# Performance work log

Measured on AMD Instinct MI355X. Metric: run time of the kernel, lower is better.

The kernel has to match this reference:

```python
import jax, jax.numpy as jnp
import numpy as np

B, N, E = 1024, 40, 64
P = N * (N - 1) // 2  # 780 field pairs


def _pair_indices(n):
    row, col = [], []
    for i in range(n - 1):
        for j in range(i + 1, n):
            row.append(i)
            col.append(j)
    return np.asarray(row), np.asarray(col)


def setup_inputs() -> dict:
    key = jax.random.key(0)
    k1, k2 = jax.random.split(key)
    inputs = jax.random.normal(k1, (B, N, E), dtype=jnp.float32)
    # xavier-normal-ish init for the 'mat' kernel (E, P, E)
    std = float(np.sqrt(2.0 / (E + E)))
    param = jax.random.normal(k2, (E, P, E), dtype=jnp.float32) * std
    return {"inputs": inputs, "param": param}


def reference(inputs, param):
    n = inputs.shape[1]
    rowidx, colidx = _pair_indices(n)
    p = inputs[:, rowidx]  # (B, P, E)
    q = inputs[:, colidx]  # (B, P, E)
    # torch: kp = (p[:,None] * param).sum(-1).transpose(1,2); out = (kp*q).sum(-1)
    # == out[b,i] = sum_{e,f} p[b,i,e] * param[f,i,e] * q[b,i,f]
    out = jnp.einsum('bie,fie,bif->bi', p, param, q)
    return out[:, None, :]  # (B, 1, P)
```

## Files before the change

### kernel.cpp

```cpp
#include <hip/hip_runtime.h>

namespace {
constexpr int kB = 1024;
constexpr int kN = 40;
constexpr int kE = 64;
constexpr int kP = kN * (kN - 1) / 2;

using bf16x8 = __attribute__((ext_vector_type(8))) short;
using f32x4  = __attribute__((ext_vector_type(4))) float;

__device__ inline unsigned short f2bf(float x) {
  union { float f; unsigned u; } v; v.f = x;
  return (unsigned short)((v.u + 0x7FFFu + ((v.u >> 16) & 1u)) >> 16);
}
__device__ inline float bf2f(unsigned short u) {
  union { unsigned u; float f; } v; v.u = (unsigned)u << 16;
  return v.f;
}

__global__ __launch_bounds__(256) void prep(const float* __restrict__ in,
                                            const float* __restrict__ param,
                                            unsigned short* __restrict__ xf,
                                            unsigned short* __restrict__ Af) {
  __shared__ short Ms[64 * 72];
  const int t = threadIdx.x;
  if (blockIdx.x < 640) {
    const int n    = blockIdx.x >> 4;
    const int bgc  = blockIdx.x & 15;
    const int bgl  = t >> 6;
    const int L    = t & 63;
    const int col  = L & 15;
    const int quad = L >> 4;
    const int b    = (bgc * 4 + bgl) * 16 + col;
    const float* src    = in + ((size_t)b * kN + n) * kE + quad * 8;
    unsigned short* dst = xf + (((size_t)n * 64 + bgc * 4 + bgl) << 10) + L * 8;
    const float4 v0 = ((const float4*)src)[0];
    const float4 v1 = ((const float4*)src)[1];
    const float4 v2 = ((const float4*)(src + 32))[0];
    const float4 v3 = ((const float4*)(src + 32))[1];
    bf16x8 o0, o1;
    o0[0] = (short)f2bf(v0.x); o0[1] = (short)f2bf(v0.y);
    o0[2] = (short)f2bf(v0.z); o0[3] = (short)f2bf(v0.w);
    o0[4] = (short)f2bf(v1.x); o0[5] = (short)f2bf(v1.y);
    o0[6] = (short)f2bf(v1.z); o0[7] = (short)f2bf(v1.w);
    o1[0] = (short)f2bf(v2.x); o1[1] = (short)f2bf(v2.y);
    o1[2] = (short)f2bf(v2.z); o1[3] = (short)f2bf(v2.w);
    o1[4] = (short)f2bf(v3.x); o1[5] = (short)f2bf(v3.y);
    o1[6] = (short)f2bf(v3.z); o1[7] = (short)f2bf(v3.w);
    *(bf16x8*)dst         = o0;
    *(bf16x8*)(dst + 512) = o1;
  } else {
    const int i = blockIdx.x - 640;
#pragma unroll
    for (int ph = 0; ph < 4; ++ph) {
      const int f  = ph * 16 + (t >> 4);
      const int e0 = (t & 15) * 4;
      const float4 v = *(const float4*)(param + ((size_t)f * kP + i) * kE + e0);
      short* d = &Ms[f * 72 + e0];
      d[0] = (short)f2bf(v.x); d[1] = (short)f2bf(v.y);
      d[2] = (short)f2bf(v.z); d[3] = (short)f2bf(v.w);
    }
    __syncthreads();
    unsigned short* base = Af + (size_t)i * 4096;
#pragma unroll
    for (int u = 0; u < 2; ++u) {
      const int chunk = t * 2 + u;
      const int L    = chunk & 63;
      const int mtks = chunk >> 6;
      const int mt   = mtks >> 1, ks = mtks & 1;
      const int col  = L & 15, quad = L >> 4;
      const bf16x8 a = *(const bf16x8*)&Ms[(16 * mt + col) * 72 + ks * 32 + quad * 8];
      *(bf16x8*)(base + chunk * 8) = a;
    }
  }
}

__global__ __launch_bounds__(256, 4)
void opn_pair2(const unsigned short* __restrict__ xf,
               const unsigned short* __restrict__ Af,
               float* __restrict__ out) {
  __shared__ float dots[256 * 2];

  const int t    = threadIdx.x;
  const int w    = t >> 6;
  const int L    = t & 63;
  const int col  = L & 15;
  const int quad = L >> 4;

  int tx = blockIdx.x, r = 0;
  for (;;) { const int nq = (40 - r) >> 1; if (tx < nq) break; tx -= nq; ++r; }
  const int c0  = r + 1 + tx * 2;
  const int ib  = r * (79 - r) / 2 + c0 - r - 1;
  const int gb0 = blockIdx.y * 256;

  const int cc = w & 1;
  const int h  = w >> 1;
  const int c  = c0 + cc;

  if (c <= kN - 1) {
    const unsigned short* ab = Af + (size_t)(ib + cc) * 4096 + L * 8;
    bf16x8 A[4][2];
#pragma unroll
    for (int mt = 0; mt < 4; ++mt)
#pragma unroll
      for (int ks = 0; ks < 2; ++ks)
        A[mt][ks] = *(const bf16x8*)(ab + (mt * 2 + ks) * 512);

    const int bgg0 = blockIdx.y * 16 + h * 8;
    const unsigned short* pb = xf + (((size_t)r * 64 + bgg0) << 10);
    const unsigned short* qb = xf + (((size_t)c * 64 + bgg0) << 10);
    const int qoff = (quad >> 1) * 128 + col * 8 + (quad & 1) * 4;

    bf16x8 B0[2], B1[2];
    ushort4 Q[2][4];
    B0[0]   = *(const bf16x8*)(pb + L * 8);
    B1[0]   = *(const bf16x8*)(pb + 512 + L * 8);
    Q[0][0] = *(const ushort4*)(qb + qoff);
    Q[0][1] = *(const ushort4*)(qb + 256 + qoff);
    Q[0][2] = *(const ushort4*)(qb + 512 + qoff);
    Q[0][3] = *(const ushort4*)(qb + 768 + qoff);

#pragma unroll
    for (int bg = 0; bg < 8; ++bg) {
      const int cb = bg & 1, nb = cb ^ 1;
      if (bg < 7) {
        const unsigned short* pn = pb + ((size_t)(bg + 1) << 10);
        const unsigned short* qn = qb + ((size_t)(bg + 1) << 10);
        B0[nb]   = *(const bf16x8*)(pn + L * 8);
        B1[nb]   = *(const bf16x8*)(pn + 512 + L * 8);
        Q[nb][0] = *(const ushort4*)(qn + qoff);
        Q[nb][1] = *(const ushort4*)(qn + 256 + qoff);
        Q[nb][2] = *(const ushort4*)(qn + 512 + qoff);
        Q[nb][3] = *(const ushort4*)(qn + 768 + qoff);
      }
      f32x4 acc[4];
#pragma unroll
      for (int mt = 0; mt < 4; ++mt) acc[mt] = (f32x4){0.f, 0.f, 0.f, 0.f};
#pragma unroll
      for (int mt = 0; mt < 4; ++mt) {
        acc[mt] = __builtin_amdgcn_mfma_f32_16x16x32_bf16(A[mt][0], B0[cb], acc[mt], 0, 0, 0);
        acc[mt] = __builtin_amdgcn_mfma_f32_16x16x32_bf16(A[mt][1], B1[cb], acc[mt], 0, 0, 0);
      }
      float s[4];
#pragma unroll
      for (int mt = 0; mt < 4; ++mt) {
        const ushort4 qu = Q[cb][mt];
        float sm;
        sm = acc[mt][0] * bf2f(qu.x);
        sm = fmaf(acc[mt][1], bf2f(qu.y), sm);
        sm = fmaf(acc[mt][2], bf2f(qu.z), sm);
        sm = fmaf(acc[mt][3], bf2f(qu.w), sm);
        s[mt] = sm;
      }
      float dot = (s[0] + s[1]) + (s[2] + s[3]);
      dot += __shfl_xor(dot, 16, 64);
      dot += __shfl_xor(dot, 32, 64);
      if (quad == 0) dots[(h * 128 + bg * 16 + col) * 2 + cc] = dot;
    }
  }
  __syncthreads();

  const float2 dv = *(const float2*)&dots[t * 2];
  float* ob = out + (size_t)(gb0 + t) * kP + ib;
  ob[0] = dv.x;
  if (c0 + 1 <= kN - 1) ob[1] = dv.y;
}

__global__ __launch_bounds__(256, 2)
void opn_fp32(const float* __restrict__ inp, const float* __restrict__ param,
              float* __restrict__ out) {
  const int i    = blockIdx.x;
  const int wave = threadIdx.x >> 6;
  const int lane = threadIdx.x & 63;
  const int b    = (blockIdx.y * 4 + wave) * 64 + lane;
  int rem = i, r = 0;
  while (rem >= kN - 1 - r) { rem -= kN - 1 - r; ++r; }
  const int c = r + 1 + rem;
  const float* pb = inp + (size_t)b * (kN * kE) + r * kE;
  const float* qb = inp + (size_t)b * (kN * kE) + c * kE;
  float p[kE];
#pragma unroll
  for (int e = 0; e < kE; ++e) p[e] = pb[e];
  float acc = 0.f;
  for (int f = 0; f < kE; ++f) {
    const float* Mrow = param + ((size_t)f * kP + i) * kE;
    float t0 = 0.f, t1 = 0.f, t2 = 0.f, t3 = 0.f;
#pragma unroll
    for (int e = 0; e < kE; e += 4) {
      t0 = fmaf(Mrow[e + 0], p[e + 0], t0);
      t1 = fmaf(Mrow[e + 1], p[e + 1], t1);
      t2 = fmaf(Mrow[e + 2], p[e + 2], t2);
      t3 = fmaf(Mrow[e + 3], p[e + 3], t3);
    }
    acc = fmaf((t0 + t1) + (t2 + t3), qb[f], acc);
  }
  out[(size_t)b * kP + i] = acc;
}
}

extern "C" void kernel_launch(void* const* d_in, const int* in_sizes, int n_in,
                              void* d_out, int out_size, void* d_ws, size_t ws_size,
                              hipStream_t stream) {
  const float* inputs = (const float*)d_in[0];
  const float* param  = (const float*)d_in[1];
  float* out          = (float*)d_out;

  const size_t xf_bytes = (size_t)kN * kB * kE * sizeof(unsigned short);
  const size_t af_bytes = (size_t)kP * 4096 * sizeof(unsigned short);

  if (ws_size >= xf_bytes + af_bytes) {
    unsigned short* xf = (unsigned short*)d_ws;
    unsigned short* Af = (unsigned short*)((char*)d_ws + xf_bytes);
    prep<<<640 + kP, 256, 0, stream>>>(inputs, param, xf, Af);
    opn_pair2<<<dim3(400, 4), 256, 0, stream>>>(xf, Af, out);
  } else {
    opn_fp32<<<dim3(kP, 4), 256, 0, stream>>>(inputs, param, out);
  }
}
```

Measured before the change: 89.38 us.

## Tile pairs as 2x4 row/column blocks per workgroup for operand reuse

The main kernel now gives each 512-thread workgroup a 2-row by 4-column tile of field pairs, one wave per pair, with each wave covering all 256 batch rows of its y-block. Before, a workgroup handled two adjacent columns of one row and split the batch range across wave halves. The aim is to let the eight waves share the same p and q field slices through cache, to cut launch count (110x4 instead of 400x4), and to write several outputs per row. In exchange, waves whose pair falls on or below the diagonal do no work, each wave runs a longer serial loop of 16 batch groups, and there are fewer workgroups to spread across the GPU.

```diff
diff --git a/kernel.cpp b/kernel.cpp
--- a/kernel.cpp
+++ b/kernel.cpp
@@ -75,11 +75,11 @@
   }
 }
 
-__global__ __launch_bounds__(256, 4)
-void opn_pair2(const unsigned short* __restrict__ xf,
+__global__ __launch_bounds__(512, 4)
+void opn_tile2(const unsigned short* __restrict__ xf,
                const unsigned short* __restrict__ Af,
                float* __restrict__ out) {
-  __shared__ float dots[256 * 2];
+  __shared__ float dots[2][256][4];
 
   const int t    = threadIdx.x;
   const int w    = t >> 6;
@@ -87,18 +87,19 @@
   const int col  = L & 15;
   const int quad = L >> 4;
 
-  int tx = blockIdx.x, r = 0;
-  for (;;) { const int nq = (40 - r) >> 1; if (tx < nq) break; tx -= nq; ++r; }
-  const int c0  = r + 1 + tx * 2;
-  const int ib  = r * (79 - r) / 2 + c0 - r - 1;
+  int a = 0, tx = blockIdx.x;
+  for (;;) { const int nb = 10 - ((2 * a + 1) >> 2); if (tx < nb) break; tx -= nb; ++a; }
+  const int cb  = ((2 * a + 1) >> 2) + tx;
+  const int r0  = 2 * a, c0 = 4 * cb;
   const int gb0 = blockIdx.y * 256;
 
-  const int cc = w & 1;
-  const int h  = w >> 1;
-  const int c  = c0 + cc;
-
-  if (c <= kN - 1) {
-    const unsigned short* ab = Af + (size_t)(ib + cc) * 4096 + L * 8;
+  const int rr = w >> 2, cc = w & 3;
+  const int r = r0 + rr, c = c0 + cc;
+
+  if (c > r) {
+    const int i = r * (79 - r) / 2 + c - r - 1;
+
+    const unsigned short* ab = Af + (size_t)i * 4096 + L * 8;
     bf16x8 A[4][2];
 #pragma unroll
     for (int mt = 0; mt < 4; ++mt)
@@ -106,7 +107,7 @@
       for (int ks = 0; ks < 2; ++ks)
         A[mt][ks] = *(const bf16x8*)(ab + (mt * 2 + ks) * 512);
 
-    const int bgg0 = blockIdx.y * 16 + h * 8;
+    const int bgg0 = blockIdx.y * 16;
     const unsigned short* pb = xf + (((size_t)r * 64 + bgg0) << 10);
     const unsigned short* qb = xf + (((size_t)c * 64 + bgg0) << 10);
     const int qoff = (quad >> 1) * 128 + col * 8 + (quad & 1) * 4;
@@ -121,30 +122,30 @@
     Q[0][3] = *(const ushort4*)(qb + 768 + qoff);
 
 #pragma unroll
-    for (int bg = 0; bg < 8; ++bg) {
-      const int cb = bg & 1, nb = cb ^ 1;
-      if (bg < 7) {
+    for (int bg = 0; bg < 16; ++bg) {
+      const int cbi = bg & 1, nbi = cbi ^ 1;
+      if (bg < 15) {
         const unsigned short* pn = pb + ((size_t)(bg + 1) << 10);
         const unsigned short* qn = qb + ((size_t)(bg + 1) << 10);
-        B0[nb]   = *(const bf16x8*)(pn + L * 8);
-        B1[nb]   = *(const bf16x8*)(pn + 512 + L * 8);
-        Q[nb][0] = *(const ushort4*)(qn + qoff);
-        Q[nb][1] = *(const ushort4*)(qn + 256 + qoff);
-        Q[nb][2] = *(const ushort4*)(qn + 512 + qoff);
-        Q[nb][3] = *(const ushort4*)(qn + 768 + qoff);
+        B0[nbi]   = *(const bf16x8*)(pn + L * 8);
+        B1[nbi]   = *(const bf16x8*)(pn + 512 + L * 8);
+        Q[nbi][0] = *(const ushort4*)(qn + qoff);
+        Q[nbi][1] = *(const ushort4*)(qn + 256 + qoff);
+        Q[nbi][2] = *(const ushort4*)(qn + 512 + qoff);
+        Q[nbi][3] = *(const ushort4*)(qn + 768 + qoff);
       }
       f32x4 acc[4];
 #pragma unroll
       for (int mt = 0; mt < 4; ++mt) acc[mt] = (f32x4){0.f, 0.f, 0.f, 0.f};
 #pragma unroll
       for (int mt = 0; mt < 4; ++mt) {
-        acc[mt] = __builtin_amdgcn_mfma_f32_16x16x32_bf16(A[mt][0], B0[cb], acc[mt], 0, 0, 0);
-        acc[mt] = __builtin_amdgcn_mfma_f32_16x16x32_bf16(A[mt][1], B1[cb], acc[mt], 0, 0, 0);
+        acc[mt] = __builtin_amdgcn_mfma_f32_16x16x32_bf16(A[mt][0], B0[cbi], acc[mt], 0, 0, 0);
+        acc[mt] = __builtin_amdgcn_mfma_f32_16x16x32_bf16(A[mt][1], B1[cbi], acc[mt], 0, 0, 0);
       }
       float s[4];
 #pragma unroll
       for (int mt = 0; mt < 4; ++mt) {
-        const ushort4 qu = Q[cb][mt];
+        const ushort4 qu = Q[cbi][mt];
         float sm;
         sm = acc[mt][0] * bf2f(qu.x);
         sm = fmaf(acc[mt][1], bf2f(qu.y), sm);
@@ -155,15 +156,22 @@
       float dot = (s[0] + s[1]) + (s[2] + s[3]);
       dot += __shfl_xor(dot, 16, 64);
       dot += __shfl_xor(dot, 32, 64);
-      if (quad == 0) dots[(h * 128 + bg * 16 + col) * 2 + cc] = dot;
+      if (quad == 0) dots[rr][bg * 16 + col][cc] = dot;
     }
   }
   __syncthreads();
 
-  const float2 dv = *(const float2*)&dots[t * 2];
-  float* ob = out + (size_t)(gb0 + t) * kP + ib;
-  ob[0] = dv.x;
-  if (c0 + 1 <= kN - 1) ob[1] = dv.y;
+  const int ob  = t >> 1;
+  const int orr = t & 1;
+  const int orx = r0 + orr;
+  const f32x4 dv = *(const f32x4*)&dots[orr][ob][0];
+  float* orow = out + (size_t)(gb0 + ob) * kP;
+  const int ibase = orx * (79 - orx) / 2 - orx - 1;
+#pragma unroll
+  for (int occ = 0; occ < 4; ++occ) {
+    const int ocp = c0 + occ;
+    if (ocp > orx) orow[ibase + ocp] = dv[occ];
+  }
 }
 
 __global__ __launch_bounds__(256, 2)
@@ -212,7 +220,7 @@
     unsigned short* xf = (unsigned short*)d_ws;
     unsigned short* Af = (unsigned short*)((char*)d_ws + xf_bytes);
     prep<<<640 + kP, 256, 0, stream>>>(inputs, param, xf, Af);
-    opn_pair2<<<dim3(400, 4), 256, 0, stream>>>(xf, Af, out);
+    opn_tile2<<<dim3(110, 4), 512, 0, stream>>>(xf, Af, out);
   } else {
     opn_fp32<<<dim3(kP, 4), 256, 0, stream>>>(inputs, param, out);
   }
```

After: 91.31 us. 2.2% more time.
